# Performance work log

Measured on AMD Instinct MI355X. Metric: run time of the kernel, lower is better.

The kernel has to match this reference:

```python
import jax, jax.numpy as jnp
import numpy as np

DIM = 256
N_EMBED = 8192


def setup_inputs() -> dict:
    key = jax.random.key(0)
    k1, k2 = jax.random.split(key)
    x = jax.random.normal(k1, (16, 32, 32, DIM), dtype=jnp.float32)
    embed = jax.random.normal(k2, (DIM, N_EMBED), dtype=jnp.float32)
    return {"x": x, "embed": embed}


def reference(x, embed):
    """VQ-VAE quantizer forward (training mode): nearest-codebook lookup,
    straight-through quantize, commitment diff, and EMA stat accumulators.
    dist uses the mm-based squared-euclidean expansion (argmin is invariant
    to the sqrt in torch.cdist)."""
    dim, n_embed = embed.shape
    flat = x.reshape(-1, dim)  # [N, dim]
    dist = (
        jnp.sum(flat * flat, axis=1, keepdims=True)
        - 2.0 * (flat @ embed)
        + jnp.sum(embed * embed, axis=0, keepdims=True)
    )
    ind = jnp.argmin(dist, axis=1)  # [N]
    # embedding gather (embed_code): embed.T is [n_embed, dim]
    quantize = jnp.take(embed.T, ind, axis=0).reshape(x.shape)
    # EMA accumulation stats (training branch):
    # embed_onehot_sum[k] = count of tokens assigned to code k
    embed_onehot_sum = jax.ops.segment_sum(
        jnp.ones_like(ind, dtype=flat.dtype), ind, num_segments=n_embed
    )  # [n_embed]
    # embed_sum = flatten.T @ onehot == segment-sum of features per code
    embed_sum = jax.ops.segment_sum(flat, ind, num_segments=n_embed).T  # [dim, n_embed]
    diff = jnp.mean((jax.lax.stop_gradient(quantize) - x) ** 2)
    quantize_st = x + jax.lax.stop_gradient(quantize - x)
    embed_ind = ind.reshape(x.shape[:-1])
    return quantize_st, diff, embed_ind, embed_onehot_sum, embed_sum
```

## Files before the change

kernel.cpp:

```cpp
#include <hip/hip_runtime.h>

#define DIM   256
#define NE    8192
#define NTOK  16384

#define OFF_Q    0
#define OFF_DIFF 4194304
#define OFF_IND  4194305
#define OFF_OH   4210689
#define OFF_ES   4218881

#define NCAND 256
#define CAP   1024
#define CHUNK 64
#define DESC_MAX 8448

typedef __attribute__((ext_vector_type(8))) short short8;
typedef __attribute__((ext_vector_type(4))) float floatx4;

__device__ inline unsigned umin2(unsigned a, unsigned b) { return a < b ? a : b; }
__device__ inline unsigned umax2(unsigned a, unsigned b) { return a > b ? a : b; }

__device__ inline void gl_lds16(const void* g, void* l) {
    __builtin_amdgcn_global_load_lds(
        (const __attribute__((address_space(1))) unsigned int*)g,
        (__attribute__((address_space(3))) unsigned int*)l, 16, 0, 0);
}

__device__ inline unsigned short b16rn(float f) {
    unsigned u = __float_as_uint(f);
    unsigned r = (u + 0x7fffu + ((u >> 16) & 1u)) >> 16;
    return (unsigned short)r;
}

__global__ void convert_x_kernel(const float* __restrict__ x,
                                 unsigned short* __restrict__ Xbf) {
    int i = blockIdx.x * 256 + threadIdx.x;
    float4 v = ((const float4*)x)[i];
    ushort4 h;
    h.x = b16rn(v.x); h.y = b16rn(v.y); h.z = b16rn(v.z); h.w = b16rn(v.w);
    ((ushort4*)Xbf)[i] = h;
}

__global__ void convert_e_kernel(const float* __restrict__ embed,
                                 unsigned short* __restrict__ EbfT,
                                 float* __restrict__ embedT,
                                 float* __restrict__ e2,
                                 float* __restrict__ es2) {
    __shared__ __align__(16) float t2[32][DIM + 4];
    __shared__ float red[32][8];
    int c0 = blockIdx.x * 32;
    int tid = threadIdx.x;
    for (int t = 0; t < 32; ++t) {
        int i = t * 256 + tid;
        int d = i >> 5, c = i & 31;
        t2[c][d] = embed[(size_t)d * NE + c0 + c];
    }
    __syncthreads();
    for (int t = 0; t < 8; ++t) {
        int i = t * 256 + tid;
        int c = i >> 6, dq = i & 63;
        float4 v = *(const float4*)&t2[c][dq * 4];
        *(float4*)&embedT[(size_t)(c0 + c) * DIM + dq * 4] = v;
        ushort4 h;
        h.x = b16rn(-512.0f * v.x); h.y = b16rn(-512.0f * v.y);
        h.z = b16rn(-512.0f * v.z); h.w = b16rn(-512.0f * v.w);
        int C = c0 + c;
        int nb = C >> 7, n = C & 127;
        size_t off = (size_t)nb * 32768 + (size_t)(dq >> 3) * 4096 +
                     (size_t)((dq >> 1) & 3) * 1024 + (size_t)n * 8 + (dq & 1) * 4;
        *(ushort4*)&EbfT[off] = h;
    }
    {
        int c = tid >> 3, seg = tid & 7;
        float s = 0.f;
        for (int d = seg * 32; d < seg * 32 + 32; ++d)
            s = fmaf(t2[c][d], t2[c][d], s);
        red[c][seg] = s;
    }
    __syncthreads();
    if (tid < 32) {
        float s = 0.f;
        for (int j = 0; j < 8; ++j) s += red[tid][j];
        e2[c0 + tid] = s;
        es2[c0 + tid] = 256.0f * (512.0f + s);
    }
}

__global__ __launch_bounds__(256, 2) void dist_screen_kernel(
    const unsigned short* __restrict__ Xbf,
    const unsigned short* __restrict__ EbfT,
    const float* __restrict__ es2,
    unsigned int* __restrict__ cand) {
    __shared__ __align__(16) unsigned short Bs[2][16384];

    const int tid  = threadIdx.x;
    const int lane = tid & 63;
    const int wid  = tid >> 6;
    const int wm   = wid >> 1, wn = wid & 1;
    const int col  = lane & 15, quad = lane >> 4;
    const int bid  = blockIdx.x;
    const int r8   = bid & 7, q8 = bid >> 3;
    const int nbg  = r8 & 3;
    const int m0   = (q8 * 2 + (r8 >> 2)) * 128;

    short8 af[4][8];
#pragma unroll
    for (int mi = 0; mi < 4; ++mi) {
        const unsigned short* base =
            Xbf + (size_t)(m0 + wm * 64 + mi * 16 + col) * DIM + quad * 8;
#pragma unroll
        for (int kb = 0; kb < 8; ++kb)
            af[mi][kb] = *(const short8*)(base + kb * 32);
    }

    unsigned b1[16], b2[16];
#pragma unroll
    for (int i = 0; i < 16; ++i) { b1[i] = 0xFFFFFFFFu; b2[i] = 0xFFFFFFFFu; }

    const char* gbase = (const char*)EbfT + (size_t)nbg * 16 * 65536 +
                        (tid >> 6) * 2048 + (tid & 63) * 16;
    char* ldst0 = (char*)Bs + tid * 16;

#define STAGE(st, b)                                                          \
    {                                                                         \
        const char* s_ = gbase + ((st) >> 1) * 65536 + ((st) & 1) * 1024;     \
        char* d_ = ldst0 + (b) * 32768;                                       \
        _Pragma("unroll")                                                     \
        for (int i_ = 0; i_ < 8; ++i_)                                        \
            gl_lds16(s_ + i_ * 8192, d_ + i_ * 4096);                         \
    }

    STAGE(0, 0);
    __syncthreads();
    int cur = 0;
    const int n_a = wn * 32 + col;
    const int n_b = wn * 32 + 16 + col;

    for (int st = 0; st < 32; ++st) {
        if (st < 31) STAGE(st + 1, cur ^ 1);

        const int n0 = nbg * 2048 + st * 64;
        float e0 = es2[n0 + n_a];
        float e1 = es2[n0 + n_b];
        floatx4 acc[4][2];
#pragma unroll
        for (int mi = 0; mi < 4; ++mi) {
            acc[mi][0] = (floatx4)e0;
            acc[mi][1] = (floatx4)e1;
        }
        const unsigned short* B = &Bs[cur][0];
#pragma unroll
        for (int kb = 0; kb < 8; ++kb) {
            short8 bf0 = *(const short8*)&B[kb * 2048 + quad * 512 + n_a * 8];
            short8 bf1 = *(const short8*)&B[kb * 2048 + quad * 512 + n_b * 8];
#pragma unroll
            for (int mi = 0; mi < 4; ++mi) {
                acc[mi][0] = __builtin_amdgcn_mfma_f32_16x16x32_bf16(
                    af[mi][kb], bf0, acc[mi][0], 0, 0, 0);
                acc[mi][1] = __builtin_amdgcn_mfma_f32_16x16x32_bf16(
                    af[mi][kb], bf1, acc[mi][1], 0, 0, 0);
            }
        }
#pragma unroll
        for (int nj = 0; nj < 2; ++nj) {
            unsigned idxc = (unsigned)(n0 + wn * 32 + nj * 16 + col);
#pragma unroll
            for (int mi = 0; mi < 4; ++mi)
#pragma unroll
                for (int r = 0; r < 4; ++r) {
                    unsigned key = ((unsigned)acc[mi][nj][r] << 13) + idxc;
                    int s = mi * 4 + r;
                    unsigned lo = umin2(key, b1[s]);
                    unsigned hi = umax2(key, b1[s]);
                    b1[s] = lo;
                    b2[s] = umin2(hi, b2[s]);
                }
        }
        __syncthreads();
        cur ^= 1;
    }
#undef STAGE

#pragma unroll
    for (int mi = 0; mi < 4; ++mi)
#pragma unroll
        for (int r = 0; r < 4; ++r) {
            int token = m0 + wm * 64 + mi * 16 + quad * 4 + r;
            uint2 v; v.x = b1[mi * 4 + r]; v.y = b2[mi * 4 + r];
            *(uint2*)&cand[(size_t)token * NCAND + nbg * 64 + wn * 32 + col * 2] = v;
        }
}

__global__ __launch_bounds__(256) void finalize_kernel(
    const float* __restrict__ x, const float* __restrict__ embedT,
    const float* __restrict__ e2,
    const unsigned int* __restrict__ cand,
    float* __restrict__ out,
    unsigned int* __restrict__ cnt,
    unsigned short* __restrict__ slots,
    float* __restrict__ diffp) {
    __shared__ float partial[4];
    int tid = threadIdx.x, w = tid >> 6, lane = tid & 63;
    int l16 = lane & 15, grp = lane >> 4;
    int token = blockIdx.x * 4 + w;

    float4 xv = *(const float4*)&x[(size_t)token * DIM + lane * 4];
    float4 xg[4];
#pragma unroll
    for (int q = 0; q < 4; ++q)
        xg[q] = *(const float4*)&x[(size_t)token * DIM + q * 64 + l16 * 4];

    float x2 = xv.x * xv.x + xv.y * xv.y + xv.z * xv.z + xv.w * xv.w;
    uint4 c = *(const uint4*)&cand[(size_t)token * NCAND + lane * 4];
    unsigned g = umin2(umin2(c.x, c.y), umin2(c.z, c.w));
#pragma unroll
    for (int m = 1; m < 64; m <<= 1) {
        x2 += __shfl_xor(x2, m);
        g = umin2(g, (unsigned)__shfl_xor((int)g, m));
    }
    const unsigned thr = g + (384u << 13);

    float bd = 3.4e38f; int bk = 0x7fffffff;
    unsigned ca[4] = {c.x, c.y, c.z, c.w};
#pragma unroll
    for (int s = 0; s < 4; ++s) {
        unsigned long long mask = __ballot(ca[s] <= thr);
        while (mask) {
            int kk[4];
#pragma unroll
            for (int g2 = 0; g2 < 4; ++g2) {
                int l = mask ? (__ffsll(mask) - 1) : 0;
                int kv = __shfl((int)ca[s], l) & 8191;
                kk[g2] = mask ? kv : -1;
                mask &= mask - 1;
            }
            int myk = kk[grp];
            int kc = myk < 0 ? 0 : myk;
            const float* er = &embedT[(size_t)kc * DIM];
            float p = 0.f;
#pragma unroll
            for (int q = 0; q < 4; ++q) {
                float4 ev = *(const float4*)&er[q * 64 + l16 * 4];
                p = fmaf(xg[q].x, ev.x, p);
                p = fmaf(xg[q].y, ev.y, p);
                p = fmaf(xg[q].z, ev.z, p);
                p = fmaf(xg[q].w, ev.w, p);
            }
#pragma unroll
            for (int m = 1; m < 16; m <<= 1) p += __shfl_xor(p, m);
            float dg = (myk >= 0) ? (e2[kc] - 2.0f * p) : 3.4e38f;
#pragma unroll
            for (int g2 = 0; g2 < 4; ++g2) {
                float d2 = __shfl(dg, g2 * 16);
                int k2 = kk[g2];
                if (k2 >= 0 && (d2 < bd || (d2 == bd && k2 < bk))) {
                    bd = d2; bk = k2;
                }
            }
        }
    }
    float4 bq = *(const float4*)&embedT[(size_t)bk * DIM + lane * 4];
    *(float4*)&out[OFF_Q + (size_t)token * DIM + lane * 4] = bq;
    if (lane == 0) {
        out[OFF_IND + token] = (float)bk;
        unsigned pos = atomicAdd(&cnt[bk], 1u);
        if (pos < CAP) slots[(size_t)bk * CAP + pos] = (unsigned short)token;
        partial[w] = x2 + bd;
    }
    __syncthreads();
    if (tid == 0)
        diffp[blockIdx.x] =
            partial[0] + partial[1] + partial[2] + partial[3];
}

__global__ __launch_bounds__(256) void build_desc_kernel(
    const unsigned int* __restrict__ cnt,
    unsigned int* __restrict__ ndesc,
    unsigned int* __restrict__ desc) {
    int k = blockIdx.x * 256 + threadIdx.x;
    int lane = threadIdx.x & 63;
    unsigned n = cnt[k];
    unsigned nc = (n > CAP) ? 1u : (n + CHUNK - 1) >> 6;
    unsigned pfx = nc;
#pragma unroll
    for (int m = 1; m < 64; m <<= 1) {
        unsigned t = __shfl_up(pfx, m);
        if (lane >= m) pfx += t;
    }
    unsigned base = 0;
    if (lane == 63) base = atomicAdd(ndesc, pfx);
    base = __shfl(base, 63);
    unsigned off = base + pfx - nc;
    for (unsigned j = 0; j < nc; ++j)
        desc[off + j] = (unsigned)k | (j << 13);
}

__global__ __launch_bounds__(256) void embed_sum_kernel(
    const float* __restrict__ x,
    const unsigned int* __restrict__ cnt,
    const unsigned short* __restrict__ slots,
    const unsigned int* __restrict__ ndesc,
    const unsigned int* __restrict__ desc,
    const float* __restrict__ out_ind,
    float* __restrict__ esT) {
    int tid = threadIdx.x, w = tid >> 6, lane = tid & 63;
    unsigned wv = blockIdx.x * 4 + w;
    if (wv >= *ndesc) return;
    unsigned dsc = desc[wv];
    int k = dsc & 8191;
    int j = dsc >> 13;
    unsigned n = cnt[k];
    float ax = 0.f, ay = 0.f, az = 0.f, aw = 0.f;

    if (n > CAP) {
        for (int tok = 0; tok < NTOK; ++tok)
            if ((int)out_ind[tok] == k) {
                float4 v = *(const float4*)&x[(size_t)tok * DIM + lane * 4];
                ax += v.x; ay += v.y; az += v.z; aw += v.w;
            }
        *(float4*)&esT[(size_t)k * DIM + lane * 4] = make_float4(ax, ay, az, aw);
        return;
    }

    int base = j * CHUNK;
    int nt = (int)n - base; if (nt > CHUNK) nt = CHUNK;
    const unsigned short* sl = &slots[(size_t)k * CAP + base];
    for (int gr = 0; gr < CHUNK; gr += 8) {
        if (gr >= nt) break;
        uint4 sv = *(const uint4*)(sl + gr);
        unsigned id[8] = {sv.x & 0xffffu, sv.x >> 16, sv.y & 0xffffu, sv.y >> 16,
                          sv.z & 0xffffu, sv.z >> 16, sv.w & 0xffffu, sv.w >> 16};
        float4 v[8];
#pragma unroll
        for (int i = 0; i < 8; ++i) {
            unsigned tok = (gr + i < nt) ? id[i] : id[0];
            v[i] = *(const float4*)&x[(size_t)tok * DIM + lane * 4];
        }
#pragma unroll
        for (int i = 0; i < 8; ++i)
            if (gr + i < nt) { ax += v[i].x; ay += v[i].y; az += v[i].z; aw += v[i].w; }
    }

    float* dst = &esT[(size_t)k * DIM + lane * 4];
    if (n <= CHUNK) {
        *(float4*)dst = make_float4(ax, ay, az, aw);
    } else {
        atomicAdd(dst + 0, ax); atomicAdd(dst + 1, ay);
        atomicAdd(dst + 2, az); atomicAdd(dst + 3, aw);
    }
}

__global__ void es_out_kernel(const float* __restrict__ esT,
                              const unsigned int* __restrict__ cnt,
                              const float* __restrict__ diffp,
                              float* __restrict__ out) {
    __shared__ __align__(16) float t2[32][DIM + 4];
    __shared__ float rsum[256];
    int k0 = blockIdx.x * 32;
    int tid = threadIdx.x;
    for (int t = 0; t < 8; ++t) {
        int i = t * 256 + tid;
        int k = i >> 6, dq = i & 63;
        float4 v = ((const float4*)esT)[(size_t)(k0 + k) * 64 + dq];
        *(float4*)&t2[k][dq * 4] = v;
    }
    __syncthreads();
    for (int t = 0; t < 32; ++t) {
        int i = t * 256 + tid;
        int d = i >> 5, c = i & 31;
        out[OFF_ES + (size_t)d * NE + k0 + c] = t2[c][d];
    }
    if (tid < 32) out[OFF_OH + k0 + tid] = (float)cnt[k0 + tid];
    if (blockIdx.x == 0) {
        float s = 0.f;
        for (int i = tid; i < NTOK / 4; i += 256) s += diffp[i];
        rsum[tid] = s;
        __syncthreads();
        for (int st = 128; st > 0; st >>= 1) {
            if (tid < st) rsum[tid] += rsum[tid + st];
            __syncthreads();
        }
        if (tid == 0) out[OFF_DIFF] = rsum[0] * (1.0f / 4194304.0f);
    }
}

extern "C" void kernel_launch(void* const* d_in, const int* in_sizes, int n_in,
                              void* d_out, int out_size, void* d_ws, size_t ws_size,
                              hipStream_t stream) {
    const float* x     = (const float*)d_in[0];
    const float* embed = (const float*)d_in[1];
    float* out = (float*)d_out;

    char* p = (char*)d_ws;
    unsigned short* Xbf  = (unsigned short*)p;  p += (size_t)NTOK * DIM * 2;
    float* esT = (float*)Xbf;
    unsigned short* EbfT = (unsigned short*)p;  p += (size_t)NE * DIM * 2;
    float* embedT = (float*)p;                  p += (size_t)NE * DIM * 4;
    float* e2     = (float*)p;                  p += (size_t)NE * 4;
    float* es2    = (float*)p;                  p += (size_t)NE * 4;
    unsigned int* cand = (unsigned int*)p;      p += (size_t)NTOK * NCAND * 4;
    unsigned int* cnt  = (unsigned int*)p;      p += (size_t)NE * 4;
    unsigned int* ndesc = (unsigned int*)p;     p += 64;
    unsigned int* desc = (unsigned int*)p;      p += (size_t)(DESC_MAX + 64) * 4;
    float* diffp = (float*)p;                   p += (size_t)(NTOK / 4) * 4;
    unsigned short* slots = (unsigned short*)p; p += (size_t)NE * CAP * 2;

    hipMemsetAsync(cnt, 0, (size_t)NE * 4 + 64, stream);

    convert_x_kernel<<<(NTOK * DIM / 4) / 256, 256, 0, stream>>>(x, Xbf);
    convert_e_kernel<<<NE / 32, 256, 0, stream>>>(embed, EbfT, embedT, e2, es2);
    dist_screen_kernel<<<512, 256, 0, stream>>>(Xbf, EbfT, es2, cand);
    finalize_kernel<<<NTOK / 4, 256, 0, stream>>>(
        x, embedT, e2, cand, out, cnt, slots, diffp);
    build_desc_kernel<<<NE / 256, 256, 0, stream>>>(cnt, ndesc, desc);
    hipMemsetAsync(esT, 0, (size_t)NE * DIM * 4, stream);
    embed_sum_kernel<<<DESC_MAX / 4, 256, 0, stream>>>(
        x, cnt, slots, ndesc, desc, out + OFF_IND, esT);
    es_out_kernel<<<NE / 32, 256, 0, stream>>>(esT, cnt, diffp, out);
}
```

Before: 186.8 us.

## Halve dist_screen tile to 64x32 per stage and double grid for occupancy

```diff
diff --git a/kernel.cpp b/kernel.cpp
--- a/kernel.cpp
+++ b/kernel.cpp
@@ -87,12 +87,12 @@
     }
 }
 
-__global__ __launch_bounds__(256, 2) void dist_screen_kernel(
+__global__ __launch_bounds__(256, 4) void dist_screen_kernel(
     const unsigned short* __restrict__ Xbf,
     const unsigned short* __restrict__ EbfT,
     const float* __restrict__ es2,
     unsigned int* __restrict__ cand) {
-    __shared__ __align__(16) unsigned short Bs[2][16384];
+    __shared__ __align__(16) unsigned short Bs[2][8192];
 
     const int tid  = threadIdx.x;
     const int lane = tid & 63;
@@ -102,91 +102,80 @@
     const int bid  = blockIdx.x;
     const int r8   = bid & 7, q8 = bid >> 3;
     const int nbg  = r8 & 3;
-    const int m0   = (q8 * 2 + (r8 >> 2)) * 128;
-
-    short8 af[4][8];
-#pragma unroll
-    for (int mi = 0; mi < 4; ++mi) {
+    const int m0   = (q8 * 2 + (r8 >> 2)) * 64;
+
+    short8 af[2][8];
+#pragma unroll
+    for (int mi = 0; mi < 2; ++mi) {
         const unsigned short* base =
-            Xbf + (size_t)(m0 + wm * 64 + mi * 16 + col) * DIM + quad * 8;
+            Xbf + (size_t)(m0 + wm * 32 + mi * 16 + col) * DIM + quad * 8;
 #pragma unroll
         for (int kb = 0; kb < 8; ++kb)
             af[mi][kb] = *(const short8*)(base + kb * 32);
     }
 
-    unsigned b1[16], b2[16];
-#pragma unroll
-    for (int i = 0; i < 16; ++i) { b1[i] = 0xFFFFFFFFu; b2[i] = 0xFFFFFFFFu; }
+    unsigned b1[8], b2[8];
+#pragma unroll
+    for (int i = 0; i < 8; ++i) { b1[i] = 0xFFFFFFFFu; b2[i] = 0xFFFFFFFFu; }
 
     const char* gbase = (const char*)EbfT + (size_t)nbg * 16 * 65536 +
-                        (tid >> 6) * 2048 + (tid & 63) * 16;
+                        (tid >> 7) * 8192 + ((tid >> 5) & 3) * 2048 +
+                        (tid & 31) * 16;
     char* ldst0 = (char*)Bs + tid * 16;
 
 #define STAGE(st, b)                                                          \
     {                                                                         \
-        const char* s_ = gbase + ((st) >> 1) * 65536 + ((st) & 1) * 1024;     \
-        char* d_ = ldst0 + (b) * 32768;                                       \
+        const char* s_ = gbase + ((st) >> 2) * 65536 + ((st) & 3) * 512;      \
+        char* d_ = ldst0 + (b) * 16384;                                       \
         _Pragma("unroll")                                                     \
-        for (int i_ = 0; i_ < 8; ++i_)                                        \
-            gl_lds16(s_ + i_ * 8192, d_ + i_ * 4096);                         \
+        for (int i_ = 0; i_ < 4; ++i_)                                        \
+            gl_lds16(s_ + i_ * 16384, d_ + i_ * 4096);                        \
     }
 
     STAGE(0, 0);
     __syncthreads();
     int cur = 0;
-    const int n_a = wn * 32 + col;
-    const int n_b = wn * 32 + 16 + col;
-
-    for (int st = 0; st < 32; ++st) {
-        if (st < 31) STAGE(st + 1, cur ^ 1);
-
-        const int n0 = nbg * 2048 + st * 64;
+    const int n_a = wn * 16 + col;
+
+    for (int st = 0; st < 64; ++st) {
+        if (st < 63) STAGE(st + 1, cur ^ 1);
+
+        const int n0 = nbg * 2048 + st * 32;
         float e0 = es2[n0 + n_a];
-        float e1 = es2[n0 + n_b];
-        floatx4 acc[4][2];
-#pragma unroll
-        for (int mi = 0; mi < 4; ++mi) {
-            acc[mi][0] = (floatx4)e0;
-            acc[mi][1] = (floatx4)e1;
+        floatx4 acc[2];
+        acc[0] = (floatx4)e0;
+        acc[1] = (floatx4)e0;
+        const unsigned short* B = &Bs[cur][0];
+#pragma unroll
+        for (int kb = 0; kb < 8; ++kb) {
+            short8 bf0 = *(const short8*)&B[kb * 1024 + quad * 256 + n_a * 8];
+            acc[0] = __builtin_amdgcn_mfma_f32_16x16x32_bf16(
+                af[0][kb], bf0, acc[0], 0, 0, 0);
+            acc[1] = __builtin_amdgcn_mfma_f32_16x16x32_bf16(
+                af[1][kb], bf0, acc[1], 0, 0, 0);
         }
-        const unsigned short* B = &Bs[cur][0];
-#pragma unroll
-        for (int kb = 0; kb < 8; ++kb) {
-            short8 bf0 = *(const short8*)&B[kb * 2048 + quad * 512 + n_a * 8];
-            short8 bf1 = *(const short8*)&B[kb * 2048 + quad * 512 + n_b * 8];
-#pragma unroll
-            for (int mi = 0; mi < 4; ++mi) {
-                acc[mi][0] = __builtin_amdgcn_mfma_f32_16x16x32_bf16(
-                    af[mi][kb], bf0, acc[mi][0], 0, 0, 0);
-                acc[mi][1] = __builtin_amdgcn_mfma_f32_16x16x32_bf16(
-                    af[mi][kb], bf1, acc[mi][1], 0, 0, 0);
+        unsigned idxc = (unsigned)(n0 + n_a);
+#pragma unroll
+        for (int mi = 0; mi < 2; ++mi)
+#pragma unroll
+            for (int r = 0; r < 4; ++r) {
+                unsigned key = ((unsigned)acc[mi][r] << 13) + idxc;
+                int s = mi * 4 + r;
+                unsigned lo = umin2(key, b1[s]);
+                unsigned hi = umax2(key, b1[s]);
+                b1[s] = lo;
+                b2[s] = umin2(hi, b2[s]);
             }
-        }
-#pragma unroll
-        for (int nj = 0; nj < 2; ++nj) {
-            unsigned idxc = (unsigned)(n0 + wn * 32 + nj * 16 + col);
-#pragma unroll
-            for (int mi = 0; mi < 4; ++mi)
-#pragma unroll
-                for (int r = 0; r < 4; ++r) {
-                    unsigned key = ((unsigned)acc[mi][nj][r] << 13) + idxc;
-                    int s = mi * 4 + r;
-                    unsigned lo = umin2(key, b1[s]);
-                    unsigned hi = umax2(key, b1[s]);
-                    b1[s] = lo;
-                    b2[s] = umin2(hi, b2[s]);
-                }
-        }
         __syncthreads();
         cur ^= 1;
     }
 #undef STAGE
 
 #pragma unroll
-    for (int mi = 0; mi < 4; ++mi)
+    for (int mi = 0; mi < 2; ++mi)
 #pragma unroll
         for (int r = 0; r < 4; ++r) {
-            int token = m0 + wm * 64 + mi * 16 + quad * 4 + r;
+            int token = m0 + wm * 32 + mi * 16 + quad * 4 + r;
             uint2 v; v.x = b1[mi * 4 + r]; v.y = b2[mi * 4 + r];
             *(uint2*)&cand[(size_t)token * NCAND + nbg * 64 + wn * 32 + col * 2] = v;
         }
@@ -410,7 +399,7 @@
 
     convert_x_kernel<<<(NTOK * DIM / 4) / 256, 256, 0, stream>>>(x, Xbf);
     convert_e_kernel<<<NE / 32, 256, 0, stream>>>(embed, EbfT, embedT, e2, es2);
-    dist_screen_kernel<<<512, 256, 0, stream>>>(Xbf, EbfT, es2, cand);
+    dist_screen_kernel<<<1024, 256, 0, stream>>>(Xbf, EbfT, es2, cand);
     finalize_kernel<<<NTOK / 4, 256, 0, stream>>>(
         x, embedT, e2, cand, out, cnt, slots, diffp);
     build_desc_kernel<<<NE / 256, 256, 0, stream>>>(cnt, ndesc, desc);
```

New measurement: 202.1 us. 8.2% more time.
